# Kernel optimization log

Hardware: AMD Instinct MI355X
Metric: run time of the kernel (lower is better)

The kernel has to match this reference:

```python
import jax, jax.numpy as jnp
import numpy as np

N, P, C, M = 64, 8732, 91, 20          # batch, n_priors (SSD300), n_classes, padded objects/image
THRESHOLD = 0.5
NEG_POS_RATIO = 3
ALPHA = 1.0


def setup_inputs() -> dict:
    key = jax.random.key(0)
    k = jax.random.split(key, 7)
    predicted_locs = jax.random.normal(k[0], (N, P, 4), jnp.float32)
    predicted_scores = jax.random.normal(k[1], (N, P, C), jnp.float32)
    # ground-truth boxes in boundary (x1,y1,x2,y2) format, valid fractional coords
    xy = jax.random.uniform(k[2], (N, M, 2), minval=0.0, maxval=0.6)
    wh = jax.random.uniform(k[3], (N, M, 2), minval=0.05, maxval=0.4)
    boxes = jnp.concatenate([xy, xy + wh], axis=-1)
    labels = jax.random.randint(k[4], (N, M), 1, C).astype(jnp.int32)  # 0 = background
    # prior boxes in center-size (cx,cy,w,h) format
    cxy = jax.random.uniform(k[5], (P, 2), minval=0.05, maxval=0.95)
    pwh = jax.random.uniform(k[6], (P, 2), minval=0.05, maxval=0.3)
    priors_cxcy = jnp.concatenate([cxy, pwh], axis=-1)
    return dict(predicted_locs=predicted_locs, predicted_scores=predicted_scores,
                boxes=boxes, labels=labels, priors_cxcy=priors_cxcy)


def _iou(a, b):
    # a: (M,4) xyxy, b: (P,4) xyxy -> (M,P)
    lo = jnp.maximum(a[:, None, :2], b[None, :, :2])
    hi = jnp.minimum(a[:, None, 2:], b[None, :, 2:])
    inter = jnp.clip(hi - lo, 0.0).prod(-1)
    area_a = (a[:, 2:] - a[:, :2]).prod(-1)
    area_b = (b[:, 2:] - b[:, :2]).prod(-1)
    return inter / (area_a[:, None] + area_b[None, :] - inter)


def _xy_to_cxcy(xy):
    return jnp.concatenate([(xy[..., :2] + xy[..., 2:]) * 0.5, xy[..., 2:] - xy[..., :2]], -1)


def _cxcy_to_gcxgcy(cxcy, priors):
    g_cxcy = (cxcy[..., :2] - priors[..., :2]) / (priors[..., 2:] / 10.0)
    g_wh = jnp.log(cxcy[..., 2:] / priors[..., 2:]) * 5.0
    return jnp.concatenate([g_cxcy, g_wh], -1)


def _match_one(boxes_i, labels_i, priors_cxcy, priors_xy):
    overlap = _iou(boxes_i, priors_xy)                    # (M, P)
    ov_per_prior = overlap.max(0)                         # (P,)
    obj_per_prior = overlap.argmax(0)                     # (P,)
    prior_per_obj = overlap.argmax(1)                     # (M,)
    # force each object onto its best prior with overlap 1
    obj_per_prior = obj_per_prior.at[prior_per_obj].set(jnp.arange(M))
    ov_per_prior = ov_per_prior.at[prior_per_obj].set(1.0)
    label_per_prior = labels_i[obj_per_prior]             # (P,)
    label_per_prior = jnp.where(ov_per_prior < THRESHOLD, 0, label_per_prior)
    true_locs = _cxcy_to_gcxgcy(_xy_to_cxcy(boxes_i[obj_per_prior]), priors_cxcy)  # (P,4)
    return label_per_prior, true_locs


def reference(predicted_locs, predicted_scores, boxes, labels, priors_cxcy):
    priors_xy = jnp.concatenate([priors_cxcy[:, :2] - priors_cxcy[:, 2:] * 0.5,
                                 priors_cxcy[:, :2] + priors_cxcy[:, 2:] * 0.5], -1)
    true_classes, true_locs = jax.vmap(_match_one, in_axes=(0, 0, None, None))(
        boxes, labels, priors_cxcy, priors_xy)            # (N,P), (N,P,4)

    pos = true_classes != 0                               # (N, P)
    n_pos = pos.sum(1)                                    # (N,)
    n_pos_total = n_pos.sum().astype(jnp.float32)

    # localization: smooth L1 (beta=1), mean over positive elements
    d = predicted_locs - true_locs
    sl1 = jnp.where(jnp.abs(d) < 1.0, 0.5 * d * d, jnp.abs(d) - 0.5)   # (N,P,4)
    loc_loss = (sl1 * pos[..., None]).sum() / (n_pos_total * 4.0)

    # confidence: per-prior cross entropy
    logp = jax.nn.log_softmax(predicted_scores, axis=-1)  # (N,P,C)
    ce = -jnp.take_along_axis(logp, true_classes[..., None], axis=-1)[..., 0]  # (N,P)

    conf_loss_pos = (ce * pos).sum()
    # hard negative mining: sort negative losses desc, take 3*n_pos per image
    ce_neg = jnp.where(pos, 0.0, ce)
    ce_neg_sorted = jnp.sort(ce_neg, axis=1)[:, ::-1]     # (N,P) descending
    hard_neg = jnp.arange(P)[None, :] < (NEG_POS_RATIO * n_pos)[:, None]
    conf_loss_hard_neg = (ce_neg_sorted * hard_neg).sum()

    conf_loss = (conf_loss_pos + conf_loss_hard_neg) / n_pos_total
    return conf_loss + ALPHA * loc_loss
```

## Files before the change

kernel.cpp:

```cpp
#include <hip/hip_runtime.h>

#define NN 64
#define PP 8732
#define CC 91
#define MM 20
#define RATIO 3
#define BPI 32
#define CHUNK 273
#define ROWS 128
#define BTHR 512
#define TILES2 ((NN * PP) / ROWS)

typedef unsigned long long u64;
typedef unsigned short u16;

__global__ __launch_bounds__(256) void match_b(
    const float4* __restrict__ boxes4,
    const float4* __restrict__ priors4,
    const int* __restrict__ labels,
    u16* __restrict__ minfo,
    u64* __restrict__ combined_part,
    int* __restrict__ counter)
{
  __shared__ float pi_s[4][CHUNK];
  __shared__ float pd_s[4][CHUNK];
  __shared__ short pm_s[4][CHUNK];
  __shared__ int lb[MM];
  const int blk = blockIdx.x, tid = threadIdx.x;
  const int wave = tid >> 6, lane = tid & 63;
  const int n = blk >> 5, part = blk & 31;
  const int c0 = part * CHUNK;
  const int cend = (c0 + CHUNK < PP) ? c0 + CHUNK : PP;
  const int clen = cend - c0;

  if (blockIdx.x == 0 && tid == 0) counter[0] = 0;
  if (tid < MM) lb[tid] = labels[n * MM + tid];

  float obx0[5], oby0[5], obx1[5], oby1[5], oba[5];
#pragma unroll
  for (int j = 0; j < 5; ++j) {
    float4 b = boxes4[n * MM + wave * 5 + j];
    obx0[j] = b.x; oby0[j] = b.y; obx1[j] = b.z; oby1[j] = b.w;
    oba[j] = (b.z - b.x) * (b.w - b.y);
  }

  float bi[5], bd[5]; int bpp[5];
#pragma unroll
  for (int j = 0; j < 5; ++j) { bi[j] = 0.0f; bd[j] = 1.0f; bpp[j] = 0; }

#pragma unroll
  for (int i = 0; i < 5; ++i) {
    int pc = lane + (i << 6);
    if (pc < clen) {
      int p = c0 + pc;
      float4 pr = priors4[p];
      float hw = pr.z * 0.5f, hh = pr.w * 0.5f;
      float px0 = pr.x - hw, py0 = pr.y - hh, px1 = pr.x + hw, py1 = pr.y + hh;
      float pa = (px1 - px0) * (py1 - py0);
      float pi = -1.0f, pd = 1.0f; int pm = 0;
#pragma unroll
      for (int j = 0; j < 5; ++j) {
        float iw = fminf(obx1[j], px1) - fmaxf(obx0[j], px0);
        float ih = fminf(oby1[j], py1) - fmaxf(oby0[j], py0);
        iw = fmaxf(iw, 0.0f); ih = fmaxf(ih, 0.0f);
        float inter = iw * ih;
        float den = (oba[j] + pa) - inter;
        bool cA = inter * pd > pi * den;
        pi = cA ? inter : pi; pd = cA ? den : pd;
        pm = cA ? (wave * 5 + j) : pm;
        bool cB = inter * bd[j] > bi[j] * den;
        bi[j] = cB ? inter : bi[j]; bd[j] = cB ? den : bd[j];
        bpp[j] = cB ? p : bpp[j];
      }
      pi_s[wave][pc] = pi; pd_s[wave][pc] = pd; pm_s[wave][pc] = (short)pm;
    }
  }

#pragma unroll
  for (int j = 0; j < 5; ++j) {
    float r = bi[j] / bd[j];
    u64 key = ((u64)__float_as_uint(r) << 32) | (unsigned)(~(unsigned)bpp[j]);
#pragma unroll
    for (int d = 1; d < 64; d <<= 1) {
      u64 o = __shfl_xor(key, d);
      key = (o > key) ? o : key;
    }
    if (lane == 0) combined_part[blk * MM + wave * 5 + j] = key;
  }
  __syncthreads();

  for (int pc = tid; pc < clen; pc += 256) {
    float pi = pi_s[0][pc], pd = pd_s[0][pc]; int pm = pm_s[0][pc];
#pragma unroll
    for (int w = 1; w < 4; ++w) {
      float qi = pi_s[w][pc], qd = pd_s[w][pc];
      bool c = qi * pd > pi * qd;
      int qm = pm_s[w][pc];
      pi = c ? qi : pi; pd = c ? qd : pd; pm = c ? qm : pm;
    }
    float q = pi / pd;
    int lab8 = (q < 0.5f) ? 0 : lb[pm];
    minfo[(size_t)n * PP + c0 + pc] = (u16)((pm << 8) | lab8);
  }
}

__global__ __launch_bounds__(BTHR) void ce_kernel(
    const float* __restrict__ scores,
    const float4* __restrict__ pred_locs4,
    const float4* __restrict__ priors4,
    const float4* __restrict__ boxes4,
    const int* __restrict__ labels,
    const u16* __restrict__ minfo,
    const u64* __restrict__ combined_part,
    float* __restrict__ ce_neg,
    float4* __restrict__ partials)
{
  __shared__ unsigned key_lo[2][MM];
  __shared__ int lbl_s[2][MM];
  __shared__ float4 box_s[2][MM];
  __shared__ float4 w8[8];
  const int tid = threadIdx.x;
  const long base = (long)blockIdx.x * ROWS;
  const int n0 = (int)(base / PP);
  const int rem0 = (int)(base - (long)n0 * PP);
  const int r = tid >> 2, l = tid & 3;
  const long row = base + r;

  const int mi = minfo[row];

  if (tid < MM) {
    const u64* cp = combined_part + (size_t)n0 * BPI * MM;
    u64 best = cp[tid];
#pragma unroll
    for (int w = 1; w < BPI; ++w) { u64 o = cp[w * MM + tid]; best = (o > best) ? o : best; }
    key_lo[0][tid] = (unsigned)best;
    lbl_s[0][tid]  = labels[n0 * MM + tid];
    box_s[0][tid]  = boxes4[n0 * MM + tid];
  } else if (tid >= 64 && tid < 64 + MM) {
    int j = tid - 64, nn = (n0 + 1 < NN) ? n0 + 1 : NN - 1;
    const u64* cp = combined_part + (size_t)nn * BPI * MM;
    u64 best = cp[j];
#pragma unroll
    for (int w = 1; w < BPI; ++w) { u64 o = cp[w * MM + j]; best = (o > best) ? o : best; }
    key_lo[1][j] = (unsigned)best;
    lbl_s[1][j]  = labels[nn * MM + j];
    box_s[1][j]  = boxes4[nn * MM + j];
  }

  const float* rp = scores + (size_t)row * CC;
  float ss0 = 0.f, ss1 = 0.f, ss2 = 0.f, ss3 = 0.f;
#pragma unroll
  for (int j = 0; j < 23; ++j) {
    int c = l + 4 * j;
    if (c < CC) {
      float e = __expf(rp[c]);
      if ((j & 3) == 0) ss0 += e;
      else if ((j & 3) == 1) ss1 += e;
      else if ((j & 3) == 2) ss2 += e;
      else ss3 += e;
    }
  }
  float s = (ss0 + ss1) + (ss2 + ss3);
  s += __shfl_xor(s, 1);
  s += __shfl_xor(s, 2);

  __syncthreads();

  float cp_ = 0.0f, lp_ = 0.0f; int pos0 = 0, pos1 = 0;
  if (l == 0) {
    const int bn = (rem0 + r >= PP) ? 1 : 0;
    const int p = rem0 + r - bn * PP;
    int mm_ = -1;
    const unsigned want = ~(unsigned)p;
#pragma unroll
    for (int j = 0; j < MM; ++j) if (key_lo[bn][j] == want) mm_ = j;
    bool pos; int lab, sm;
    if (mm_ >= 0) { pos = true; sm = mm_; lab = lbl_s[bn][mm_]; }
    else { lab = mi & 0xff; pos = (lab != 0); sm = mi >> 8; }
    float ce = __logf(s) - rp[lab];
    if (pos) {
      cp_ = ce; ce_neg[row] = 0.0f;
      if (bn) pos1 = 1; else pos0 = 1;
      float4 bx = box_s[bn][sm], pr = priors4[p], pl = pred_locs4[row];
      float cx = (bx.x + bx.z) * 0.5f, cy = (bx.y + bx.w) * 0.5f;
      float w = bx.z - bx.x, h = bx.w - bx.y;
      float gx = (cx - pr.x) / (pr.z / 10.0f);
      float gy = (cy - pr.y) / (pr.w / 10.0f);
      float gz = __logf(w / pr.z) * 5.0f;
      float gw = __logf(h / pr.w) * 5.0f;
      float d, a;
      d = pl.x - gx; a = fabsf(d); lp_ += (a < 1.0f) ? 0.5f * d * d : a - 0.5f;
      d = pl.y - gy; a = fabsf(d); lp_ += (a < 1.0f) ? 0.5f * d * d : a - 0.5f;
      d = pl.z - gz; a = fabsf(d); lp_ += (a < 1.0f) ? 0.5f * d * d : a - 0.5f;
      d = pl.w - gw; a = fabsf(d); lp_ += (a < 1.0f) ? 0.5f * d * d : a - 0.5f;
    } else {
      ce_neg[row] = fmaxf(ce, 0.0f);
    }
  }

#pragma unroll
  for (int d = 1; d < 64; d <<= 1) {
    cp_ += __shfl_xor(cp_, d); lp_ += __shfl_xor(lp_, d);
    pos0 += __shfl_xor(pos0, d); pos1 += __shfl_xor(pos1, d);
  }
  if ((tid & 63) == 0)
    w8[tid >> 6] = make_float4(cp_, lp_, (float)pos0, (float)pos1);
  __syncthreads();
  if (tid == 0) {
    float sx = 0.f, sy = 0.f, sz = 0.f, sw = 0.f;
#pragma unroll
    for (int w = 0; w < 8; ++w) { sx += w8[w].x; sy += w8[w].y; sz += w8[w].z; sw += w8[w].w; }
    partials[blockIdx.x] = make_float4(sx, sy, sz, sw);
  }
}

__global__ __launch_bounds__(256) void hardneg_kernel(
    const float* __restrict__ ce_neg, const float4* __restrict__ partials,
    float4* __restrict__ per_img, int* __restrict__ counter,
    float* __restrict__ out)
{
  __shared__ int4 cred[2][4];
  __shared__ float wredf[4];
  __shared__ int wcnt[4];
  __shared__ float4 wacc[4];
  __shared__ int last_s;
  const int n = blockIdx.x, tid = threadIdx.x;

  unsigned uv[35];
#pragma unroll
  for (int i = 0; i < 35; ++i) {
    int p = tid + (i << 8);
    uv[i] = (p < PP) ? __float_as_uint(ce_neg[(size_t)n * PP + p]) : 0u;
  }

  float kc = 0.0f, cpo = 0.0f, lpo = 0.0f;
  {
    const int bstart = (n * PP) / ROWS;
    const int bend = ((n + 1) * PP - 1) / ROWS;
    const int ost = (n * PP + ROWS - 1) / ROWS;
    const int oen = ((n + 1) * PP + ROWS - 1) / ROWS;
    for (int b = bstart + tid; b <= bend; b += 256) {
      float4 pb = partials[b];
      int nb0 = (b * ROWS) / PP;
      if (nb0 == n)     kc += pb.z;
      if (nb0 + 1 == n) kc += pb.w;
      if (b >= ost && b < oen) { cpo += pb.x; lpo += pb.y; }
    }
#pragma unroll
    for (int d = 1; d < 64; d <<= 1) {
      kc += __shfl_xor(kc, d); cpo += __shfl_xor(cpo, d); lpo += __shfl_xor(lpo, d);
    }
    if ((tid & 63) == 0) wacc[tid >> 6] = make_float4(kc, cpo, lpo, 0.f);
    __syncthreads();
    kc = wacc[0].x + wacc[1].x + wacc[2].x + wacc[3].x;
    cpo = wacc[0].y + wacc[1].y + wacc[2].y + wacc[3].y;
    lpo = wacc[0].z + wacc[1].z + wacc[2].z + wacc[3].z;
  }
  const float npn = kc;
  const int k = RATIO * (int)(kc + 0.5f);

  float hs = 0.0f;
  if (k >= PP) {
    float s = 0.0f;
#pragma unroll
    for (int i = 0; i < 35; ++i) s += __uint_as_float(uv[i]);
#pragma unroll
    for (int d = 1; d < 64; d <<= 1) s += __shfl_xor(s, d);
    __syncthreads();
    if ((tid & 63) == 0) wredf[tid >> 6] = s;
    __syncthreads();
    hs = wredf[0] + wredf[1] + wredf[2] + wredf[3];
  } else if (k > 0) {
    unsigned lo = 0u, hi = 0x7f7fffffu;
    int it = 0;
    while (lo < hi) {
      unsigned span = hi - lo;
      unsigned q4 = span >> 2;
      unsigned m1, m2, m3;
      if (q4 == 0) { m1 = m2 = m3 = lo + ((span + 1) >> 1); }
      else { m1 = lo + q4; m2 = lo + 2 * q4; m3 = lo + 3 * q4; }
      int a1 = 0, a2 = 0, a3 = 0;
#pragma unroll
      for (int i = 0; i < 35; ++i) {
        unsigned v = uv[i];
        a1 += (v >= m1); a2 += (v >= m2); a3 += (v >= m3);
      }
#pragma unroll
      for (int d = 1; d < 64; d <<= 1) {
        a1 += __shfl_xor(a1, d); a2 += __shfl_xor(a2, d); a3 += __shfl_xor(a3, d);
      }
      const int buf = it & 1;
      if ((tid & 63) == 0) cred[buf][tid >> 6] = make_int4(a1, a2, a3, 0);
      __syncthreads();
      int c1 = 0, c2 = 0, c3 = 0;
#pragma unroll
      for (int w = 0; w < 4; ++w) {
        int4 cc = cred[buf][w];
        c1 += cc.x; c2 += cc.y; c3 += cc.z;
      }
      if (c3 >= k) lo = m3;
      else if (c2 >= k) { lo = m2; hi = m3 - 1; }
      else if (c1 >= k) { lo = m1; hi = m2 - 1; }
      else hi = m1 - 1;
      ++it;
    }
    const float x = __uint_as_float(lo);
    float s = 0.0f; int c = 0;
#pragma unroll
    for (int i = 0; i < 35; ++i) {
      unsigned v = uv[i];
      if (v > lo) { s += __uint_as_float(v); ++c; }
    }
#pragma unroll
    for (int d = 1; d < 64; d <<= 1) { s += __shfl_xor(s, d); c += __shfl_xor(c, d); }
    __syncthreads();
    if ((tid & 63) == 0) { wredf[tid >> 6] = s; wcnt[tid >> 6] = c; }
    __syncthreads();
    hs = (wredf[0] + wredf[1] + wredf[2] + wredf[3]) +
         (float)(k - (wcnt[0] + wcnt[1] + wcnt[2] + wcnt[3])) * x;
  }

  if (tid == 0) {
    per_img[n] = make_float4(cpo, lpo, npn, hs);
    __threadfence();
    last_s = atomicAdd(counter, 1);
  }
  __syncthreads();
  if (last_s == NN - 1) {
    __threadfence();
    if (tid < 64) {
      float4 v = per_img[tid];
      float a = v.x, b = v.y, c = v.z, d = v.w;
#pragma unroll
      for (int dd = 1; dd < 64; dd <<= 1) {
        a += __shfl_xor(a, dd); b += __shfl_xor(b, dd);
        c += __shfl_xor(c, dd); d += __shfl_xor(d, dd);
      }
      if (tid == 0) out[0] = (a + d) / c + b / (c * 4.0f);
    }
  }
}

extern "C" void kernel_launch(void* const* d_in, const int* in_sizes, int n_in,
                              void* d_out, int out_size, void* d_ws, size_t ws_size,
                              hipStream_t stream) {
  const float*  pred_locs   = (const float*)d_in[0];
  const float*  pred_scores = (const float*)d_in[1];
  const float*  boxes       = (const float*)d_in[2];
  const int*    labels      = (const int*)d_in[3];
  const float*  priors      = (const float*)d_in[4];
  float* out = (float*)d_out;

  u16* minfo = (u16*)d_ws;
  float4* partials = (float4*)(minfo + (size_t)NN * PP);
  float*  ce_neg = (float*)(partials + TILES2);
  u64* combined_part = (u64*)(ce_neg + (size_t)NN * PP);
  float4* per_img = (float4*)(combined_part + (size_t)NN * BPI * MM);
  int* counter = (int*)(per_img + NN);

  match_b<<<NN * BPI, 256, 0, stream>>>((const float4*)boxes,
                                        (const float4*)priors, labels,
                                        minfo, combined_part, counter);
  ce_kernel<<<TILES2, BTHR, 0, stream>>>(pred_scores,
                                         (const float4*)pred_locs,
                                         (const float4*)priors,
                                         (const float4*)boxes, labels,
                                         minfo, combined_part,
                                         ce_neg, partials);
  hardneg_kernel<<<NN, 256, 0, stream>>>(ce_neg, partials, per_img,
                                         counter, out);
}
```

Before: 81.68 us.

## Move per-prior best-object matching into CE kernel and add separate key reduction

The per-prior argmax over objects now happens inside the cross-entropy kernel, which computes IoU against the shared-memory boxes across 4 lanes. This removes the minfo intermediate array and the shared-memory stage from the match kernel, which now only tracks the best prior per object. A small new kernel reduces the per-block keys once per image, so CE blocks no longer each re-reduce 32 partials. The hard-negative kernel also loads ce_neg with uint4 vector loads. The trade-off is one extra kernel launch and some extra ALU work in the CE kernel.

```diff
diff --git a/kernel.cpp b/kernel.cpp
--- a/kernel.cpp
+++ b/kernel.cpp
@@ -12,29 +12,20 @@
 #define TILES2 ((NN * PP) / ROWS)
 
 typedef unsigned long long u64;
-typedef unsigned short u16;
-
-__global__ __launch_bounds__(256) void match_b(
+
+__global__ __launch_bounds__(256) void match_lite(
     const float4* __restrict__ boxes4,
     const float4* __restrict__ priors4,
-    const int* __restrict__ labels,
-    u16* __restrict__ minfo,
     u64* __restrict__ combined_part,
     int* __restrict__ counter)
 {
-  __shared__ float pi_s[4][CHUNK];
-  __shared__ float pd_s[4][CHUNK];
-  __shared__ short pm_s[4][CHUNK];
-  __shared__ int lb[MM];
   const int blk = blockIdx.x, tid = threadIdx.x;
   const int wave = tid >> 6, lane = tid & 63;
   const int n = blk >> 5, part = blk & 31;
   const int c0 = part * CHUNK;
   const int cend = (c0 + CHUNK < PP) ? c0 + CHUNK : PP;
-  const int clen = cend - c0;
-
-  if (blockIdx.x == 0 && tid == 0) counter[0] = 0;
-  if (tid < MM) lb[tid] = labels[n * MM + tid];
+
+  if (blk == 0 && tid == 0) counter[0] = 0;
 
   float obx0[5], oby0[5], obx1[5], oby1[5], oba[5];
 #pragma unroll
@@ -43,21 +34,19 @@
     obx0[j] = b.x; oby0[j] = b.y; obx1[j] = b.z; oby1[j] = b.w;
     oba[j] = (b.z - b.x) * (b.w - b.y);
   }
-
   float bi[5], bd[5]; int bpp[5];
 #pragma unroll
   for (int j = 0; j < 5; ++j) { bi[j] = 0.0f; bd[j] = 1.0f; bpp[j] = 0; }
 
 #pragma unroll
   for (int i = 0; i < 5; ++i) {
-    int pc = lane + (i << 6);
-    if (pc < clen) {
-      int p = c0 + pc;
+    int p = c0 + lane + (i << 6);
+    if (p < cend) {
       float4 pr = priors4[p];
       float hw = pr.z * 0.5f, hh = pr.w * 0.5f;
-      float px0 = pr.x - hw, py0 = pr.y - hh, px1 = pr.x + hw, py1 = pr.y + hh;
+      float px0 = pr.x - hw, py0 = pr.y - hh;
+      float px1 = pr.x + hw, py1 = pr.y + hh;
       float pa = (px1 - px0) * (py1 - py0);
-      float pi = -1.0f, pd = 1.0f; int pm = 0;
 #pragma unroll
       for (int j = 0; j < 5; ++j) {
         float iw = fminf(obx1[j], px1) - fmaxf(obx0[j], px0);
@@ -65,14 +54,10 @@
         iw = fmaxf(iw, 0.0f); ih = fmaxf(ih, 0.0f);
         float inter = iw * ih;
         float den = (oba[j] + pa) - inter;
-        bool cA = inter * pd > pi * den;
-        pi = cA ? inter : pi; pd = cA ? den : pd;
-        pm = cA ? (wave * 5 + j) : pm;
-        bool cB = inter * bd[j] > bi[j] * den;
-        bi[j] = cB ? inter : bi[j]; bd[j] = cB ? den : bd[j];
-        bpp[j] = cB ? p : bpp[j];
-      }
-      pi_s[wave][pc] = pi; pd_s[wave][pc] = pd; pm_s[wave][pc] = (short)pm;
+        bool c = inter * bd[j] > bi[j] * den;
+        bi[j] = c ? inter : bi[j]; bd[j] = c ? den : bd[j];
+        bpp[j] = c ? p : bpp[j];
+      }
     }
   }
 
@@ -87,20 +72,26 @@
     }
     if (lane == 0) combined_part[blk * MM + wave * 5 + j] = key;
   }
-  __syncthreads();
-
-  for (int pc = tid; pc < clen; pc += 256) {
-    float pi = pi_s[0][pc], pd = pd_s[0][pc]; int pm = pm_s[0][pc];
-#pragma unroll
-    for (int w = 1; w < 4; ++w) {
-      float qi = pi_s[w][pc], qd = pd_s[w][pc];
-      bool c = qi * pd > pi * qd;
-      int qm = pm_s[w][pc];
-      pi = c ? qi : pi; pd = c ? qd : pd; pm = c ? qm : pm;
-    }
-    float q = pi / pd;
-    int lab8 = (q < 0.5f) ? 0 : lb[pm];
-    minfo[(size_t)n * PP + c0 + pc] = (u16)((pm << 8) | lab8);
+}
+
+__global__ __launch_bounds__(192) void reduce_kernel(
+    const u64* __restrict__ combined_part, u64* __restrict__ combined)
+{
+  const int n = blockIdx.x, tid = threadIdx.x;
+  if (tid < 160) {
+    const int j = tid >> 3, w = tid & 7;
+    const u64* cp = combined_part + (size_t)n * BPI * MM;
+    u64 best = 0;
+#pragma unroll
+    for (int k = 0; k < 4; ++k) {
+      u64 o = cp[(w * 4 + k) * MM + j];
+      best = (o > best) ? o : best;
+    }
+    u64 o;
+    o = __shfl_down(best, 4, 8); best = (o > best) ? o : best;
+    o = __shfl_down(best, 2, 8); best = (o > best) ? o : best;
+    o = __shfl_down(best, 1, 8); best = (o > best) ? o : best;
+    if (w == 0) combined[n * MM + j] = best;
   }
 }
 
@@ -110,8 +101,7 @@
     const float4* __restrict__ priors4,
     const float4* __restrict__ boxes4,
     const int* __restrict__ labels,
-    const u16* __restrict__ minfo,
-    const u64* __restrict__ combined_part,
+    const u64* __restrict__ combined,
     float* __restrict__ ce_neg,
     float4* __restrict__ partials)
 {
@@ -126,23 +116,13 @@
   const int r = tid >> 2, l = tid & 3;
   const long row = base + r;
 
-  const int mi = minfo[row];
-
   if (tid < MM) {
-    const u64* cp = combined_part + (size_t)n0 * BPI * MM;
-    u64 best = cp[tid];
-#pragma unroll
-    for (int w = 1; w < BPI; ++w) { u64 o = cp[w * MM + tid]; best = (o > best) ? o : best; }
-    key_lo[0][tid] = (unsigned)best;
+    key_lo[0][tid] = (unsigned)combined[n0 * MM + tid];
     lbl_s[0][tid]  = labels[n0 * MM + tid];
     box_s[0][tid]  = boxes4[n0 * MM + tid];
   } else if (tid >= 64 && tid < 64 + MM) {
     int j = tid - 64, nn = (n0 + 1 < NN) ? n0 + 1 : NN - 1;
-    const u64* cp = combined_part + (size_t)nn * BPI * MM;
-    u64 best = cp[j];
-#pragma unroll
-    for (int w = 1; w < BPI; ++w) { u64 o = cp[w * MM + j]; best = (o > best) ? o : best; }
-    key_lo[1][j] = (unsigned)best;
+    key_lo[1][j] = (unsigned)combined[nn * MM + j];
     lbl_s[1][j]  = labels[nn * MM + j];
     box_s[1][j]  = boxes4[nn * MM + j];
   }
@@ -166,28 +146,63 @@
 
   __syncthreads();
 
+  const int bn = (rem0 + r >= PP) ? 1 : 0;
+  const int p = rem0 + r - bn * PP;
+  const float4 pr4 = priors4[p];
+  float bi, bd; int bm;
+  {
+    float hw = pr4.z * 0.5f, hh = pr4.w * 0.5f;
+    float px0 = pr4.x - hw, py0 = pr4.y - hh;
+    float px1 = pr4.x + hw, py1 = pr4.y + hh;
+    float pa = (px1 - px0) * (py1 - py0);
+    bi = -1.0f; bd = 1.0f; bm = l;
+#pragma unroll
+    for (int j5 = 0; j5 < 5; ++j5) {
+      int m = l + 4 * j5;
+      float4 bx = box_s[bn][m];
+      float iw = fminf(bx.z, px1) - fmaxf(bx.x, px0);
+      float ih = fminf(bx.w, py1) - fmaxf(bx.y, py0);
+      iw = fmaxf(iw, 0.0f); ih = fmaxf(ih, 0.0f);
+      float inter = iw * ih;
+      float ba = (bx.z - bx.x) * (bx.w - bx.y);
+      float den = (ba + pa) - inter;
+      bool c = inter * bd > bi * den;
+      bi = c ? inter : bi; bd = c ? den : bd; bm = c ? m : bm;
+    }
+#pragma unroll
+    for (int d = 1; d < 4; d <<= 1) {
+      float oi = __shfl_xor(bi, d), od = __shfl_xor(bd, d);
+      int om = __shfl_xor(bm, d);
+      float a = oi * bd, b2 = bi * od;
+      bool take = (a > b2) || (a == b2 && om < bm);
+      bi = take ? oi : bi; bd = take ? od : bd; bm = take ? om : bm;
+    }
+  }
+
   float cp_ = 0.0f, lp_ = 0.0f; int pos0 = 0, pos1 = 0;
   if (l == 0) {
-    const int bn = (rem0 + r >= PP) ? 1 : 0;
-    const int p = rem0 + r - bn * PP;
     int mm_ = -1;
     const unsigned want = ~(unsigned)p;
 #pragma unroll
     for (int j = 0; j < MM; ++j) if (key_lo[bn][j] == want) mm_ = j;
     bool pos; int lab, sm;
     if (mm_ >= 0) { pos = true; sm = mm_; lab = lbl_s[bn][mm_]; }
-    else { lab = mi & 0xff; pos = (lab != 0); sm = mi >> 8; }
+    else {
+      float q = bi / bd;
+      pos = !(q < 0.5f);
+      sm = bm; lab = pos ? lbl_s[bn][bm] : 0;
+    }
     float ce = __logf(s) - rp[lab];
     if (pos) {
       cp_ = ce; ce_neg[row] = 0.0f;
       if (bn) pos1 = 1; else pos0 = 1;
-      float4 bx = box_s[bn][sm], pr = priors4[p], pl = pred_locs4[row];
+      float4 bx = box_s[bn][sm], pl = pred_locs4[row];
       float cx = (bx.x + bx.z) * 0.5f, cy = (bx.y + bx.w) * 0.5f;
       float w = bx.z - bx.x, h = bx.w - bx.y;
-      float gx = (cx - pr.x) / (pr.z / 10.0f);
-      float gy = (cy - pr.y) / (pr.w / 10.0f);
-      float gz = __logf(w / pr.z) * 5.0f;
-      float gw = __logf(h / pr.w) * 5.0f;
+      float gx = (cx - pr4.x) / (pr4.z / 10.0f);
+      float gy = (cy - pr4.y) / (pr4.w / 10.0f);
+      float gz = __logf(w / pr4.z) * 5.0f;
+      float gw = __logf(h / pr4.w) * 5.0f;
       float d, a;
       d = pl.x - gx; a = fabsf(d); lp_ += (a < 1.0f) ? 0.5f * d * d : a - 0.5f;
       d = pl.y - gy; a = fabsf(d); lp_ += (a < 1.0f) ? 0.5f * d * d : a - 0.5f;
@@ -226,11 +241,14 @@
   __shared__ int last_s;
   const int n = blockIdx.x, tid = threadIdx.x;
 
-  unsigned uv[35];
-#pragma unroll
-  for (int i = 0; i < 35; ++i) {
-    int p = tid + (i << 8);
-    uv[i] = (p < PP) ? __float_as_uint(ce_neg[(size_t)n * PP + p]) : 0u;
+  uint4 uv[9];
+  {
+    const uint4* cn4 = (const uint4*)(ce_neg + (size_t)n * PP);
+#pragma unroll
+    for (int i = 0; i < 9; ++i) {
+      int f = tid + (i << 8);
+      uv[i] = (f < 2183) ? cn4[f] : make_uint4(0u, 0u, 0u, 0u);
+    }
   }
 
   float kc = 0.0f, cpo = 0.0f, lpo = 0.0f;
@@ -248,11 +266,12 @@
     }
 #pragma unroll
     for (int d = 1; d < 64; d <<= 1) {
-      kc += __shfl_xor(kc, d); cpo += __shfl_xor(cpo, d); lpo += __shfl_xor(lpo, d);
+      kc += __shfl_xor(kc, d); cpo += __shfl_xor(cpo, d);
+      lpo += __shfl_xor(lpo, d);
     }
     if ((tid & 63) == 0) wacc[tid >> 6] = make_float4(kc, cpo, lpo, 0.f);
     __syncthreads();
-    kc = wacc[0].x + wacc[1].x + wacc[2].x + wacc[3].x;
+    kc  = wacc[0].x + wacc[1].x + wacc[2].x + wacc[3].x;
     cpo = wacc[0].y + wacc[1].y + wacc[2].y + wacc[3].y;
     lpo = wacc[0].z + wacc[1].z + wacc[2].z + wacc[3].z;
   }
@@ -263,7 +282,10 @@
   if (k >= PP) {
     float s = 0.0f;
 #pragma unroll
-    for (int i = 0; i < 35; ++i) s += __uint_as_float(uv[i]);
+    for (int i = 0; i < 9; ++i) {
+      s += __uint_as_float(uv[i].x) + __uint_as_float(uv[i].y) +
+           __uint_as_float(uv[i].z) + __uint_as_float(uv[i].w);
+    }
 #pragma unroll
     for (int d = 1; d < 64; d <<= 1) s += __shfl_xor(s, d);
     __syncthreads();
@@ -281,9 +303,10 @@
       else { m1 = lo + q4; m2 = lo + 2 * q4; m3 = lo + 3 * q4; }
       int a1 = 0, a2 = 0, a3 = 0;
 #pragma unroll
-      for (int i = 0; i < 35; ++i) {
-        unsigned v = uv[i];
-        a1 += (v >= m1); a2 += (v >= m2); a3 += (v >= m3);
+      for (int i = 0; i < 9; ++i) {
+        a1 += (uv[i].x >= m1) + (uv[i].y >= m1) + (uv[i].z >= m1) + (uv[i].w >= m1);
+        a2 += (uv[i].x >= m2) + (uv[i].y >= m2) + (uv[i].z >= m2) + (uv[i].w >= m2);
+        a3 += (uv[i].x >= m3) + (uv[i].y >= m3) + (uv[i].z >= m3) + (uv[i].w >= m3);
       }
 #pragma unroll
       for (int d = 1; d < 64; d <<= 1) {
@@ -307,9 +330,11 @@
     const float x = __uint_as_float(lo);
     float s = 0.0f; int c = 0;
 #pragma unroll
-    for (int i = 0; i < 35; ++i) {
-      unsigned v = uv[i];
-      if (v > lo) { s += __uint_as_float(v); ++c; }
+    for (int i = 0; i < 9; ++i) {
+      if (uv[i].x > lo) { s += __uint_as_float(uv[i].x); ++c; }
+      if (uv[i].y > lo) { s += __uint_as_float(uv[i].y); ++c; }
+      if (uv[i].z > lo) { s += __uint_as_float(uv[i].z); ++c; }
+      if (uv[i].w > lo) { s += __uint_as_float(uv[i].w); ++c; }
     }
 #pragma unroll
     for (int d = 1; d < 64; d <<= 1) { s += __shfl_xor(s, d); c += __shfl_xor(c, d); }
@@ -351,22 +376,22 @@
   const float*  priors      = (const float*)d_in[4];
   float* out = (float*)d_out;
 
-  u16* minfo = (u16*)d_ws;
-  float4* partials = (float4*)(minfo + (size_t)NN * PP);
+  float4* partials = (float4*)d_ws;
   float*  ce_neg = (float*)(partials + TILES2);
   u64* combined_part = (u64*)(ce_neg + (size_t)NN * PP);
-  float4* per_img = (float4*)(combined_part + (size_t)NN * BPI * MM);
+  u64* combined = combined_part + (size_t)NN * BPI * MM;
+  float4* per_img = (float4*)(combined + NN * MM);
   int* counter = (int*)(per_img + NN);
 
-  match_b<<<NN * BPI, 256, 0, stream>>>((const float4*)boxes,
-                                        (const float4*)priors, labels,
-                                        minfo, combined_part, counter);
+  match_lite<<<NN * BPI, 256, 0, stream>>>((const float4*)boxes,
+                                           (const float4*)priors,
+                                           combined_part, counter);
+  reduce_kernel<<<NN, 192, 0, stream>>>(combined_part, combined);
   ce_kernel<<<TILES2, BTHR, 0, stream>>>(pred_scores,
                                          (const float4*)pred_locs,
                                          (const float4*)priors,
                                          (const float4*)boxes, labels,
-                                         minfo, combined_part,
-                                         ce_neg, partials);
+                                         combined, ce_neg, partials);
   hardneg_kernel<<<NN, 256, 0, stream>>>(ce_neg, partials, per_img,
                                          counter, out);
 }
```

Measured after the change: 82.78 us. About the same (+1.3%).
